# Kernel optimization log

Hardware: AMD Instinct MI355X
Metric: run time of the kernel (lower is better)

The kernel has to match this reference:

```python
import jax, jax.numpy as jnp
import numpy as np

DIM = 768
NUM_EXPERTS = 1536
EXPERT_DIM = 64
NOISE_SCALE = 0.1
B, H, W = 1, 64, 64
N = B * H * W


def setup_inputs() -> dict:
    key = jax.random.key(0)
    ks = jax.random.split(key, 6)
    scaled = lambda k, shape, fan_in: (jax.random.normal(k, shape, jnp.float32) / np.sqrt(fan_in)).astype(jnp.float32)
    return {
        "x": jax.random.normal(ks[0], (B, H, W, DIM), jnp.float32),
        "noise": jax.random.normal(ks[1], (N, NUM_EXPERTS), jnp.float32),
        "gate_w": scaled(ks[2], (NUM_EXPERTS, DIM), DIM),
        "gate_b": jnp.zeros((NUM_EXPERTS,), jnp.float32),
        "expert_w": scaled(ks[3], (NUM_EXPERTS, EXPERT_DIM, DIM), DIM),  # torch Linear weight layout (out, in)
        "expert_b": jnp.zeros((NUM_EXPERTS, EXPERT_DIM), jnp.float32),
        "proj_w": scaled(ks[4], (DIM, EXPERT_DIM), EXPERT_DIM),
        "proj_b": jnp.zeros((DIM,), jnp.float32),
    }


def reference(x, noise, gate_w, gate_b, expert_w, expert_b, proj_w, proj_b):
    orig_shape = x.shape
    xf = x.reshape(-1, orig_shape[-1])  # (N, DIM)
    # Noisy gating
    scores = xf @ gate_w.T + gate_b + noise * NOISE_SCALE  # (N, E)
    gate_weights = jax.nn.softmax(scores, axis=-1)
    top_w, top_i = jax.lax.top_k(gate_weights, 1)  # (N, 1), (N, 1)
    idx = top_i[:, 0]  # (N,)
    # Gather only the selected expert per token (same math as the redundant
    # dense all-expert compute followed by a gather in the original).
    w_sel = expert_w[idx]  # (N, EXPERT_DIM, DIM)
    b_sel = expert_b[idx]  # (N, EXPERT_DIM)
    y = jnp.einsum('nd,nod->no', xf, w_sel) + b_sel  # (N, EXPERT_DIM)
    out_flat = (y @ proj_w.T + proj_b) * top_w  # (N, DIM); top_w broadcasts (N,1)
    return out_flat.reshape(orig_shape)
```

## Files before the change

kernel.cpp:

```cpp
#include <hip/hip_runtime.h>
#include <hip/hip_bf16.h>

#define NT 4096
#define DIM 768
#define NE 1536
#define ED 64
#define GAP_THR 8e-3f
#define MAXG 2304

typedef __attribute__((ext_vector_type(8))) short short8v;
typedef __attribute__((ext_vector_type(4))) float f32x4;

__device__ __forceinline__ unsigned short f2bf(float f) {
  unsigned int u = __float_as_uint(f);
  unsigned int r = (u + 0x7fffu + ((u >> 16) & 1u)) >> 16;
  return (unsigned short)r;
}
__device__ __forceinline__ float bf2f(unsigned short h) {
  return __uint_as_float(((unsigned int)h) << 16);
}

__device__ __forceinline__ void gload16(const void* g, void* l) {
  __builtin_amdgcn_global_load_lds((const __attribute__((address_space(1))) void*)g,
                                   (__attribute__((address_space(3))) void*)l, 16, 0, 0);
}

__device__ __forceinline__ void top2_merge(float& m1, int& i1, float& m2, int& i2,
                                           float om1, int oi1, float om2, int oi2) {
  if (om1 > m1 || (om1 == m1 && oi1 < i1)) {
    if (m1 > om2 || (m1 == om2 && i1 < oi2)) { m2 = m1; i2 = i1; }
    else { m2 = om2; i2 = oi2; }
    m1 = om1; i1 = oi1;
  } else {
    if (om1 > m2 || (om1 == m2 && oi1 < i2)) { m2 = om1; i2 = oi1; }
  }
}

__global__ __launch_bounds__(256) void split_all(
    const float* __restrict__ x, const float* __restrict__ gw,
    unsigned short* __restrict__ xhi, unsigned short* __restrict__ xlo,
    unsigned short* __restrict__ ghi, unsigned short* __restrict__ glo,
    int* __restrict__ rc_cnt, int* __restrict__ counts) {
  if (blockIdx.x == 0) {
    for (int j = threadIdx.x; j < NE; j += 256) counts[j] = 0;
    if (threadIdx.x == 0) *rc_cnt = 0;
  }
  const int nx4 = NT * DIM / 4;
  const int ng4 = NE * DIM / 4;
  int i = blockIdx.x * 256 + threadIdx.x;
  const float* src; unsigned short* hi; unsigned short* lo; int j;
  if (i < nx4) { src = x; hi = xhi; lo = xlo; j = i; }
  else { j = i - nx4; if (j >= ng4) return; src = gw; hi = ghi; lo = glo; }
  float4 v = ((const float4*)src)[j];
  unsigned short h0 = f2bf(v.x), h1 = f2bf(v.y), h2 = f2bf(v.z), h3 = f2bf(v.w);
  ((ushort4*)hi)[j] = make_ushort4(h0, h1, h2, h3);
  ((ushort4*)lo)[j] = make_ushort4(f2bf(v.x - bf2f(h0)), f2bf(v.y - bf2f(h1)),
                                   f2bf(v.z - bf2f(h2)), f2bf(v.w - bf2f(h3)));
}

__global__ __launch_bounds__(256) void gate_mfma(
    const unsigned short* __restrict__ xhi, const unsigned short* __restrict__ xlo,
    const unsigned short* __restrict__ ghi, const unsigned short* __restrict__ glo,
    const float* __restrict__ gb, const float* __restrict__ noise,
    float4* __restrict__ part_a, int* __restrict__ part_i2) {
  __shared__ __align__(16) unsigned short sA[2 * 64 * 32];
  __shared__ __align__(16) unsigned short sB[2 * 128 * 32];
  const int tid = threadIdx.x;
  const int w = tid >> 6, lane = tid & 63;
  const int bm = blockIdx.x, bn = blockIdx.y;
  const int fr = lane & 15;
  const int fg = lane >> 4;
  const int gsw = fg ^ ((fr >> 1) & 3);

  f32x4 acc[4][2];
#pragma unroll
  for (int i = 0; i < 4; i++)
#pragma unroll
    for (int j = 0; j < 2; j++) acc[i][j] = (f32x4){0.f, 0.f, 0.f, 0.f};

  const size_t arow = (size_t)bm * 64 * DIM;
  const size_t brow = (size_t)bn * 128 * DIM;
  const int rA = tid >> 2;
  const int sgA = (tid & 3) ^ ((rA >> 1) & 3);
  const int sgB = (tid & 3) ^ ((tid >> 3) & 3);

  for (int kt = 0; kt < DIM; kt += 32) {
    __syncthreads();
    {
      const size_t asrc = arow + (size_t)rA * DIM + kt + sgA * 8;
      gload16(xhi + asrc, &sA[w * 512]);
      gload16(xlo + asrc, &sA[2048 + w * 512]);
#pragma unroll
      for (int h = 0; h < 2; h++) {
        const int r = h * 64 + (tid >> 2);
        const size_t bsrc = brow + (size_t)r * DIM + kt + sgB * 8;
        gload16(ghi + bsrc, &sB[h * 2048 + w * 512]);
        gload16(glo + bsrc, &sB[4096 + h * 2048 + w * 512]);
      }
    }
    __syncthreads();

    short8v ah[4], al[4], bh[2], bl[2];
#pragma unroll
    for (int mf = 0; mf < 4; mf++) {
      int ro = (mf * 16 + fr) * 32 + gsw * 8;
      ah[mf] = *(const short8v*)&sA[ro];
      al[mf] = *(const short8v*)&sA[2048 + ro];
    }
#pragma unroll
    for (int nf = 0; nf < 2; nf++) {
      int ro = (w * 32 + nf * 16 + fr) * 32 + gsw * 8;
      bh[nf] = *(const short8v*)&sB[ro];
      bl[nf] = *(const short8v*)&sB[4096 + ro];
    }
#pragma unroll
    for (int mf = 0; mf < 4; mf++)
#pragma unroll
      for (int nf = 0; nf < 2; nf++) {
        f32x4 c = acc[mf][nf];
        c = __builtin_amdgcn_mfma_f32_16x16x32_bf16(ah[mf], bh[nf], c, 0, 0, 0);
        c = __builtin_amdgcn_mfma_f32_16x16x32_bf16(ah[mf], bl[nf], c, 0, 0, 0);
        c = __builtin_amdgcn_mfma_f32_16x16x32_bf16(al[mf], bh[nf], c, 0, 0, 0);
        acc[mf][nf] = c;
      }
  }

  const int gm0 = bm * 64;
  const int gn0 = bn * 128 + w * 32;
  const int chunk = bn * 4 + w;
  int gcol[2]; float gbv[2];
#pragma unroll
  for (int nf = 0; nf < 2; nf++) { gcol[nf] = gn0 + nf * 16 + fr; gbv[nf] = gb[gcol[nf]]; }
#pragma unroll
  for (int mf = 0; mf < 4; mf++) {
    float sv[2][4];
#pragma unroll
    for (int nf = 0; nf < 2; nf++)
#pragma unroll
      for (int reg = 0; reg < 4; reg++) {
        int gm = gm0 + mf * 16 + fg * 4 + reg;
        sv[nf][reg] = acc[mf][nf][reg] + gbv[nf] + 0.1f * noise[(size_t)gm * NE + gcol[nf]];
      }
#pragma unroll
    for (int reg = 0; reg < 4; reg++) {
      float m1 = sv[0][reg]; int i1 = gcol[0];
      float m2 = -3e38f; int i2 = 0x7fffffff;
      {
        float v = sv[1][reg]; int ii = gcol[1];
        if (v > m1 || (v == m1 && ii < i1)) { m2 = m1; i2 = i1; m1 = v; i1 = ii; }
        else { m2 = v; i2 = ii; }
      }
#pragma unroll
      for (int off = 1; off <= 8; off <<= 1) {
        float om1 = __shfl_xor(m1, off, 64); int oi1 = __shfl_xor(i1, off, 64);
        float om2 = __shfl_xor(m2, off, 64); int oi2 = __shfl_xor(i2, off, 64);
        top2_merge(m1, i1, m2, i2, om1, oi1, om2, oi2);
      }
      float ssum = __expf(sv[0][reg] - m1) + __expf(sv[1][reg] - m1);
#pragma unroll
      for (int off = 1; off <= 8; off <<= 1) ssum += __shfl_xor(ssum, off, 64);
      if (fr == 0) {
        int gm = gm0 + mf * 16 + fg * 4 + reg;
        part_a[(size_t)gm * 48 + chunk] = make_float4(m1, m2, ssum, __int_as_float(i1));
        part_i2[(size_t)gm * 48 + chunk] = i2;
      }
    }
  }
}

__global__ __launch_bounds__(256) void finalize(
    const float4* __restrict__ part_a, const int* __restrict__ part_i2,
    float* __restrict__ topw, int* __restrict__ idx, int* __restrict__ counts,
    int* __restrict__ rc_count, int* __restrict__ rc_n, int* __restrict__ rc_i2) {
  const int wv = threadIdx.x >> 6, lane = threadIdx.x & 63;
  const int n = blockIdx.x * 4 + wv;
  float m1 = -3e38f, m2 = -3e38f, lm1 = -3e38f, lsum = 0.f;
  int i1 = 0x7fffffff, i2 = 0x7fffffff;
  if (lane < 48) {
    float4 pa = part_a[(size_t)n * 48 + lane];
    m1 = pa.x; m2 = pa.y; lsum = pa.z; i1 = __float_as_int(pa.w);
    i2 = part_i2[(size_t)n * 48 + lane];
    lm1 = pa.x;
  }
#pragma unroll
  for (int off = 1; off <= 32; off <<= 1) {
    float om1 = __shfl_xor(m1, off, 64); int oi1 = __shfl_xor(i1, off, 64);
    float om2 = __shfl_xor(m2, off, 64); int oi2 = __shfl_xor(i2, off, 64);
    top2_merge(m1, i1, m2, i2, om1, oi1, om2, oi2);
  }
  float contrib = (lane < 48) ? __expf(lm1 - m1) * lsum : 0.f;
#pragma unroll
  for (int off = 1; off <= 32; off <<= 1) contrib += __shfl_xor(contrib, off, 64);
  if (lane == 0) {
    topw[n] = 1.0f / contrib;
    idx[n] = i1;
    atomicAdd(counts + i1, 1);
    if (m1 - m2 < GAP_THR) {
      int p = atomicAdd(rc_count, 1);
      rc_n[p] = n; rc_i2[p] = i2;
    }
  }
}

__global__ __launch_bounds__(256) void recheck(
    const float* __restrict__ x, const float* __restrict__ gw,
    const float* __restrict__ gb, const float* __restrict__ noise,
    const int* __restrict__ rc_n, const int* __restrict__ rc_i2,
    const int* __restrict__ rc_count, int* __restrict__ idx, int* __restrict__ counts) {
  __shared__ float r1[4], r2[4];
  const int cnt = *rc_count;
  const int tid = threadIdx.x;
  const int w = tid >> 6, lane = tid & 63;
  for (int t = blockIdx.x; t < cnt; t += gridDim.x) {
    const int n = rc_n[t];
    const int e1 = idx[n], e2 = rc_i2[t];
    const float* xr = x + (size_t)n * DIM;
    const float* w1 = gw + (size_t)e1 * DIM;
    const float* w2 = gw + (size_t)e2 * DIM;
    float p1 = 0.f, p2 = 0.f;
    for (int k = tid; k < DIM; k += 256) {
      float xv = xr[k];
      p1 += xv * w1[k];
      p2 += xv * w2[k];
    }
#pragma unroll
    for (int off = 32; off; off >>= 1) {
      p1 += __shfl_xor(p1, off, 64);
      p2 += __shfl_xor(p2, off, 64);
    }
    if (lane == 0) { r1[w] = p1; r2[w] = p2; }
    __syncthreads();
    if (tid == 0) {
      float s1 = r1[0] + r1[1] + r1[2] + r1[3] + gb[e1] + 0.1f * noise[(size_t)n * NE + e1];
      float s2 = r2[0] + r2[1] + r2[2] + r2[3] + gb[e2] + 0.1f * noise[(size_t)n * NE + e2];
      if (s2 > s1 || (s2 == s1 && e2 < e1)) {
        idx[n] = e2;
        atomicSub(counts + e1, 1);
        atomicAdd(counts + e2, 1);
      }
    }
    __syncthreads();
  }
}

__global__ __launch_bounds__(256) void scan_offsets(
    const int* __restrict__ counts, int* __restrict__ offs, int* __restrict__ cursor,
    int* __restrict__ gdesc, int* __restrict__ ngroups) {
  __shared__ int part[256];
  __shared__ int part2[256];
  const int t = threadIdx.x;
  int loc[6];
  int s = 0, s2 = 0;
#pragma unroll
  for (int j = 0; j < 6; j++) {
    loc[j] = counts[t * 6 + j];
    s += loc[j];
    s2 += (loc[j] + 3) >> 2;
  }
  part[t] = s; part2[t] = s2;
  __syncthreads();
  for (int d = 1; d < 256; d <<= 1) {
    int v1 = (t >= d) ? part[t - d] : 0;
    int v2 = (t >= d) ? part2[t - d] : 0;
    __syncthreads();
    part[t] += v1; part2[t] += v2;
    __syncthreads();
  }
  int excl = part[t] - s;
  int excl2 = part2[t] - s2;
#pragma unroll
  for (int j = 0; j < 6; j++) {
    const int e = t * 6 + j, c = loc[j];
    offs[e] = excl;
    cursor[e] = excl;
    const int ng = (c + 3) >> 2;
    for (int k = 0; k < ng; k++) {
      gdesc[3 * (excl2 + k)]     = e;
      gdesc[3 * (excl2 + k) + 1] = excl + 4 * k;
      gdesc[3 * (excl2 + k) + 2] = min(4, c - 4 * k);
    }
    excl += c; excl2 += ng;
  }
  if (t == 255) *ngroups = part2[255];
}

__global__ __launch_bounds__(256) void scatter_tokens(
    const int* __restrict__ idx, int* __restrict__ cursor, int* __restrict__ sorted) {
  const int n = blockIdx.x * 256 + threadIdx.x;
  int e = idx[n];
  int pos = atomicAdd(cursor + e, 1);
  sorted[pos] = n;
}

__global__ __launch_bounds__(256) void expert_y(
    const float* __restrict__ x, const float* __restrict__ ew,
    const float* __restrict__ eb, const int* __restrict__ sorted,
    const int* __restrict__ gdesc, const int* __restrict__ ngroups,
    float* __restrict__ y) {
  const int g = blockIdx.x;
  if (g >= *ngroups) return;
  const int e    = gdesc[3 * g];
  const int base = gdesc[3 * g + 1];
  const int cc   = gdesc[3 * g + 2];
  const int tid = threadIdx.x;
  const int w = tid >> 6, lane = tid & 63;

  const int tk0 = sorted[base];
  const int tk1 = sorted[base + (1 < cc ? 1 : 0)];
  const int tk2 = sorted[base + (2 < cc ? 2 : 0)];
  const int tk3 = sorted[base + (3 < cc ? 3 : 0)];
  const int mytk = (lane == 0) ? tk0 : (lane == 1) ? tk1 : (lane == 2) ? tk2 : tk3;

  const float4* W4 = (const float4*)(ew + (size_t)e * ED * DIM);
  const float4* X4 = (const float4*)x;
  const float4* Wc = W4 + w * 16 * 192;

  f32x4 x00 = *(const f32x4*)&X4[(size_t)tk0 * 192 + lane];
  f32x4 x01 = *(const f32x4*)&X4[(size_t)tk0 * 192 + 64 + lane];
  f32x4 x02 = *(const f32x4*)&X4[(size_t)tk0 * 192 + 128 + lane];
  f32x4 x10 = *(const f32x4*)&X4[(size_t)tk1 * 192 + lane];
  f32x4 x11 = *(const f32x4*)&X4[(size_t)tk1 * 192 + 64 + lane];
  f32x4 x12 = *(const f32x4*)&X4[(size_t)tk1 * 192 + 128 + lane];
  f32x4 x20 = *(const f32x4*)&X4[(size_t)tk2 * 192 + lane];
  f32x4 x21 = *(const f32x4*)&X4[(size_t)tk2 * 192 + 64 + lane];
  f32x4 x22 = *(const f32x4*)&X4[(size_t)tk2 * 192 + 128 + lane];
  f32x4 x30 = *(const f32x4*)&X4[(size_t)tk3 * 192 + lane];
  f32x4 x31 = *(const f32x4*)&X4[(size_t)tk3 * 192 + 64 + lane];
  f32x4 x32 = *(const f32x4*)&X4[(size_t)tk3 * 192 + 128 + lane];

  f32x4 wbuf[2][3];
#pragma unroll
  for (int j = 0; j < 3; j++) wbuf[0][j] = *(const f32x4*)&Wc[j * 64 + lane];
#pragma unroll
  for (int j = 0; j < 3; j++) wbuf[1][j] = *(const f32x4*)&Wc[192 + j * 64 + lane];

#pragma unroll
  for (int a = 0; a < 16; a++) {
    const int cur = a & 1;
    f32x4 wa0 = wbuf[cur][0], wa1 = wbuf[cur][1], wa2 = wbuf[cur][2];
    if (a < 14) {
      wbuf[cur][0] = *(const f32x4*)&Wc[(a + 2) * 192 + lane];
      wbuf[cur][1] = *(const f32x4*)&Wc[(a + 2) * 192 + 64 + lane];
      wbuf[cur][2] = *(const f32x4*)&Wc[(a + 2) * 192 + 128 + lane];
    }
    float p0 = wa0.x * x00.x + wa0.y * x00.y + wa0.z * x00.z + wa0.w * x00.w
             + wa1.x * x01.x + wa1.y * x01.y + wa1.z * x01.z + wa1.w * x01.w
             + wa2.x * x02.x + wa2.y * x02.y + wa2.z * x02.z + wa2.w * x02.w;
    float p1 = wa0.x * x10.x + wa0.y * x10.y + wa0.z * x10.z + wa0.w * x10.w
             + wa1.x * x11.x + wa1.y * x11.y + wa1.z * x11.z + wa1.w * x11.w
             + wa2.x * x12.x + wa2.y * x12.y + wa2.z * x12.z + wa2.w * x12.w;
    float p2 = wa0.x * x20.x + wa0.y * x20.y + wa0.z * x20.z + wa0.w * x20.w
             + wa1.x * x21.x + wa1.y * x21.y + wa1.z * x21.z + wa1.w * x21.w
             + wa2.x * x22.x + wa2.y * x22.y + wa2.z * x22.z + wa2.w * x22.w;
    float p3 = wa0.x * x30.x + wa0.y * x30.y + wa0.z * x30.z + wa0.w * x30.w
             + wa1.x * x31.x + wa1.y * x31.y + wa1.z * x31.z + wa1.w * x31.w
             + wa2.x * x32.x + wa2.y * x32.y + wa2.z * x32.z + wa2.w * x32.w;

    const bool b0 = (lane & 1) != 0;
    float q0 = (b0 ? p1 : p0) + __shfl_xor(b0 ? p0 : p1, 1, 64);
    float q1 = (b0 ? p3 : p2) + __shfl_xor(b0 ? p2 : p3, 1, 64);
    const bool b1 = (lane & 2) != 0;
    float r = (b1 ? q1 : q0) + __shfl_xor(b1 ? q0 : q1, 2, 64);
    r += __shfl_xor(r, 4, 64);
    r += __shfl_xor(r, 8, 64);
    r += __shfl_xor(r, 16, 64);
    r += __shfl_xor(r, 32, 64);

    const int o = w * 16 + a;
    if (lane < cc) {
      y[(size_t)mytk * ED + o] = r + eb[e * ED + o];
    }
  }
}

__global__ __launch_bounds__(256) void proj_kernel(
    const float* __restrict__ y, const float* __restrict__ pw,
    const float* __restrict__ pb, const float* __restrict__ topw,
    float* __restrict__ out) {
  const int b = blockIdx.x;
  const int tid = threadIdx.x;
  __shared__ float4 ys4[8 * 16];
  __shared__ float tw[8];
  if (tid < 128) {
    int t = tid >> 4, q = tid & 15;
    ys4[tid] = ((const float4*)y)[((size_t)b * 8 + t) * 16 + q];
  }
  if (tid < 8) tw[tid] = topw[b * 8 + tid];
  __syncthreads();
  const float4* pw4 = (const float4*)pw;
#pragma unroll
  for (int c = 0; c < 3; c++) {
    int d = c * 256 + tid;
    float4 pwv[16];
#pragma unroll
    for (int q = 0; q < 16; q++) pwv[q] = pw4[(size_t)d * 16 + q];
    float pbv = pb[d];
    for (int t = 0; t < 8; t++) {
      const float4* yv4 = &ys4[t * 16];
      float s = 0.f;
#pragma unroll
      for (int q = 0; q < 16; q++) {
        float4 yv = yv4[q];
        s += pwv[q].x * yv.x + pwv[q].y * yv.y + pwv[q].z * yv.z + pwv[q].w * yv.w;
      }
      out[((size_t)b * 8 + t) * DIM + d] = (s + pbv) * tw[t];
    }
  }
}

extern "C" void kernel_launch(void* const* d_in, const int* in_sizes, int n_in,
                              void* d_out, int out_size, void* d_ws, size_t ws_size,
                              hipStream_t stream) {
  const float* x      = (const float*)d_in[0];
  const float* noise  = (const float*)d_in[1];
  const float* gate_w = (const float*)d_in[2];
  const float* gate_b = (const float*)d_in[3];
  const float* ew     = (const float*)d_in[4];
  const float* eb     = (const float*)d_in[5];
  const float* pw     = (const float*)d_in[6];
  const float* pb     = (const float*)d_in[7];
  float* out = (float*)d_out;

  char* ws = (char*)d_ws;
  unsigned short* xhi    = (unsigned short*)(ws);
  unsigned short* xlo    = (unsigned short*)(ws + 6291456);
  unsigned short* ghi    = (unsigned short*)(ws + 12582912);
  unsigned short* glo    = (unsigned short*)(ws + 14942208);
  float4*         part_a = (float4*)(ws + 17301504);
  int*            part_i2= (int*)  (ws + 20447232);
  float*          y      = (float*)(ws + 21233664);
  float*          topw   = (float*)(ws + 22282240);
  int*            idx    = (int*)  (ws + 22298624);
  int*            counts = (int*)  (ws + 22315008);
  int*            rc_cnt = (int*)  (ws + 22321152);
  int*            offs   = (int*)  (ws + 22321408);
  int*            cursor = (int*)  (ws + 22327552);
  int*            sorted = (int*)  (ws + 22333696);
  int*            rc_n   = (int*)  (ws + 22350080);
  int*            rc_i2  = (int*)  (ws + 22366464);
  int*            ngroups= (int*)  (ws + 22382848);
  int*            gdesc  = (int*)  (ws + 22383104);

  split_all<<<(NT * DIM / 4 + NE * DIM / 4 + 255) / 256, 256, 0, stream>>>(
      x, gate_w, xhi, xlo, ghi, glo, rc_cnt, counts);
  gate_mfma<<<dim3(NT / 64, NE / 128), 256, 0, stream>>>(
      xhi, xlo, ghi, glo, gate_b, noise, part_a, part_i2);
  finalize<<<NT / 4, 256, 0, stream>>>(part_a, part_i2, topw, idx, counts,
                                       rc_cnt, rc_n, rc_i2);
  recheck<<<64, 256, 0, stream>>>(x, gate_w, gate_b, noise, rc_n, rc_i2, rc_cnt,
                                  idx, counts);
  scan_offsets<<<1, 256, 0, stream>>>(counts, offs, cursor, gdesc, ngroups);
  scatter_tokens<<<NT / 256, 256, 0, stream>>>(idx, cursor, sorted);
  expert_y<<<MAXG, 256, 0, stream>>>(x, ew, eb, sorted, gdesc, ngroups, y);
  proj_kernel<<<NT / 8, 256, 0, stream>>>(y, pw, pb, topw, out);
}
```

Baseline: 232.4 us.

## Use fp16 split gate GEMM with double-buffered LDS and fused scan/scatter

The gate GEMM now uses fp16: x is stored as a single fp16 copy and gate_w as an fp16 hi/lo pair. This cuts the split-precision MFMAs from three to two per fragment and removes the x low-part buffer traffic. The K loop double-buffers LDS so the next tile loads while the current one computes, with one barrier per iteration. The scan_offsets and scatter_tokens kernels are merged into one single-block kernel that uses LDS atomics, removing one launch. The risks are fp16 range and precision loss on x, which the recheck gap threshold must absorb, and a serial scatter running on only one block.

```diff
diff --git a/kernel.cpp b/kernel.cpp
--- a/kernel.cpp
+++ b/kernel.cpp
@@ -8,17 +8,9 @@
 #define GAP_THR 8e-3f
 #define MAXG 2304
 
-typedef __attribute__((ext_vector_type(8))) short short8v;
+typedef __attribute__((ext_vector_type(8))) _Float16 half8v;
+typedef __attribute__((ext_vector_type(4))) _Float16 half4v;
 typedef __attribute__((ext_vector_type(4))) float f32x4;
-
-__device__ __forceinline__ unsigned short f2bf(float f) {
-  unsigned int u = __float_as_uint(f);
-  unsigned int r = (u + 0x7fffu + ((u >> 16) & 1u)) >> 16;
-  return (unsigned short)r;
-}
-__device__ __forceinline__ float bf2f(unsigned short h) {
-  return __uint_as_float(((unsigned int)h) << 16);
-}
 
 __device__ __forceinline__ void gload16(const void* g, void* l) {
   __builtin_amdgcn_global_load_lds((const __attribute__((address_space(1))) void*)g,
@@ -38,8 +30,7 @@
 
 __global__ __launch_bounds__(256) void split_all(
     const float* __restrict__ x, const float* __restrict__ gw,
-    unsigned short* __restrict__ xhi, unsigned short* __restrict__ xlo,
-    unsigned short* __restrict__ ghi, unsigned short* __restrict__ glo,
+    _Float16* __restrict__ xh, _Float16* __restrict__ gh, _Float16* __restrict__ gl,
     int* __restrict__ rc_cnt, int* __restrict__ counts) {
   if (blockIdx.x == 0) {
     for (int j = threadIdx.x; j < NE; j += 256) counts[j] = 0;
@@ -48,28 +39,34 @@
   const int nx4 = NT * DIM / 4;
   const int ng4 = NE * DIM / 4;
   int i = blockIdx.x * 256 + threadIdx.x;
-  const float* src; unsigned short* hi; unsigned short* lo; int j;
-  if (i < nx4) { src = x; hi = xhi; lo = xlo; j = i; }
-  else { j = i - nx4; if (j >= ng4) return; src = gw; hi = ghi; lo = glo; }
-  float4 v = ((const float4*)src)[j];
-  unsigned short h0 = f2bf(v.x), h1 = f2bf(v.y), h2 = f2bf(v.z), h3 = f2bf(v.w);
-  ((ushort4*)hi)[j] = make_ushort4(h0, h1, h2, h3);
-  ((ushort4*)lo)[j] = make_ushort4(f2bf(v.x - bf2f(h0)), f2bf(v.y - bf2f(h1)),
-                                   f2bf(v.z - bf2f(h2)), f2bf(v.w - bf2f(h3)));
+  if (i < nx4) {
+    float4 v = ((const float4*)x)[i];
+    half4v hv = {(_Float16)v.x, (_Float16)v.y, (_Float16)v.z, (_Float16)v.w};
+    ((half4v*)xh)[i] = hv;
+  } else {
+    int j = i - nx4;
+    if (j >= ng4) return;
+    float4 v = ((const float4*)gw)[j];
+    half4v hv = {(_Float16)v.x, (_Float16)v.y, (_Float16)v.z, (_Float16)v.w};
+    half4v lv = {(_Float16)(v.x - (float)hv[0]), (_Float16)(v.y - (float)hv[1]),
+                 (_Float16)(v.z - (float)hv[2]), (_Float16)(v.w - (float)hv[3])};
+    ((half4v*)gh)[j] = hv;
+    ((half4v*)gl)[j] = lv;
+  }
 }
 
 __global__ __launch_bounds__(256) void gate_mfma(
-    const unsigned short* __restrict__ xhi, const unsigned short* __restrict__ xlo,
-    const unsigned short* __restrict__ ghi, const unsigned short* __restrict__ glo,
-    const float* __restrict__ gb, const float* __restrict__ noise,
-    float4* __restrict__ part_a, int* __restrict__ part_i2) {
-  __shared__ __align__(16) unsigned short sA[2 * 64 * 32];
-  __shared__ __align__(16) unsigned short sB[2 * 128 * 32];
+    const _Float16* __restrict__ xh, const _Float16* __restrict__ gh,
+    const _Float16* __restrict__ gl, const float* __restrict__ gb,
+    const float* __restrict__ noise, float4* __restrict__ part_a,
+    int* __restrict__ part_i2) {
+  __shared__ __align__(16) _Float16 sA[2][64 * 32];
+  __shared__ __align__(16) _Float16 sBh[2][128 * 32];
+  __shared__ __align__(16) _Float16 sBl[2][128 * 32];
   const int tid = threadIdx.x;
   const int w = tid >> 6, lane = tid & 63;
   const int bm = blockIdx.x, bn = blockIdx.y;
-  const int fr = lane & 15;
-  const int fg = lane >> 4;
+  const int fr = lane & 15, fg = lane >> 4;
   const int gsw = fg ^ ((fr >> 1) & 3);
 
   f32x4 acc[4][2];
@@ -81,49 +78,47 @@
   const size_t arow = (size_t)bm * 64 * DIM;
   const size_t brow = (size_t)bn * 128 * DIM;
   const int rA = tid >> 2;
-  const int sgA = (tid & 3) ^ ((rA >> 1) & 3);
-  const int sgB = (tid & 3) ^ ((tid >> 3) & 3);
-
-  for (int kt = 0; kt < DIM; kt += 32) {
-    __syncthreads();
-    {
-      const size_t asrc = arow + (size_t)rA * DIM + kt + sgA * 8;
-      gload16(xhi + asrc, &sA[w * 512]);
-      gload16(xlo + asrc, &sA[2048 + w * 512]);
-#pragma unroll
-      for (int h = 0; h < 2; h++) {
-        const int r = h * 64 + (tid >> 2);
-        const size_t bsrc = brow + (size_t)r * DIM + kt + sgB * 8;
-        gload16(ghi + bsrc, &sB[h * 2048 + w * 512]);
-        gload16(glo + bsrc, &sB[4096 + h * 2048 + w * 512]);
-      }
-    }
-    __syncthreads();
-
-    short8v ah[4], al[4], bh[2], bl[2];
-#pragma unroll
-    for (int mf = 0; mf < 4; mf++) {
-      int ro = (mf * 16 + fr) * 32 + gsw * 8;
-      ah[mf] = *(const short8v*)&sA[ro];
-      al[mf] = *(const short8v*)&sA[2048 + ro];
-    }
+  const int sg = (tid & 3) ^ ((rA >> 1) & 3);
+  const int dA = w * 512;
+
+#define STAGE(b, kt) do {                                                     \
+    gload16(xh + arow + (size_t)rA * DIM + (kt) + sg * 8, &sA[b][dA]);        \
+    gload16(gh + brow + (size_t)rA * DIM + (kt) + sg * 8, &sBh[b][dA]);       \
+    gload16(gl + brow + (size_t)rA * DIM + (kt) + sg * 8, &sBl[b][dA]);       \
+    gload16(gh + brow + (size_t)(64 + rA) * DIM + (kt) + sg * 8, &sBh[b][2048 + dA]); \
+    gload16(gl + brow + (size_t)(64 + rA) * DIM + (kt) + sg * 8, &sBl[b][2048 + dA]); \
+  } while (0)
+
+  STAGE(0, 0);
+  __syncthreads();
+
+  for (int t = 0; t < 24; t++) {
+    const int cur = t & 1;
+    if (t < 23) {
+      if (cur) STAGE(0, (t + 1) * 32); else STAGE(1, (t + 1) * 32);
+    }
+    half8v a8[4], b8h[2], b8l[2];
+#pragma unroll
+    for (int mf = 0; mf < 4; mf++)
+      a8[mf] = *(const half8v*)&sA[cur][(mf * 16 + fr) * 32 + gsw * 8];
 #pragma unroll
     for (int nf = 0; nf < 2; nf++) {
       int ro = (w * 32 + nf * 16 + fr) * 32 + gsw * 8;
-      bh[nf] = *(const short8v*)&sB[ro];
-      bl[nf] = *(const short8v*)&sB[4096 + ro];
+      b8h[nf] = *(const half8v*)&sBh[cur][ro];
+      b8l[nf] = *(const half8v*)&sBl[cur][ro];
     }
 #pragma unroll
     for (int mf = 0; mf < 4; mf++)
 #pragma unroll
       for (int nf = 0; nf < 2; nf++) {
         f32x4 c = acc[mf][nf];
-        c = __builtin_amdgcn_mfma_f32_16x16x32_bf16(ah[mf], bh[nf], c, 0, 0, 0);
-        c = __builtin_amdgcn_mfma_f32_16x16x32_bf16(ah[mf], bl[nf], c, 0, 0, 0);
-        c = __builtin_amdgcn_mfma_f32_16x16x32_bf16(al[mf], bh[nf], c, 0, 0, 0);
+        c = __builtin_amdgcn_mfma_f32_16x16x32_f16(a8[mf], b8h[nf], c, 0, 0, 0);
+        c = __builtin_amdgcn_mfma_f32_16x16x32_f16(a8[mf], b8l[nf], c, 0, 0, 0);
         acc[mf][nf] = c;
       }
-  }
+    __syncthreads();
+  }
+#undef STAGE
 
   const int gm0 = bm * 64;
   const int gn0 = bn * 128 + w * 32;
@@ -243,11 +238,12 @@
   }
 }
 
-__global__ __launch_bounds__(256) void scan_offsets(
-    const int* __restrict__ counts, int* __restrict__ offs, int* __restrict__ cursor,
-    int* __restrict__ gdesc, int* __restrict__ ngroups) {
+__global__ __launch_bounds__(256) void sortscan(
+    const int* __restrict__ counts, const int* __restrict__ idx,
+    int* __restrict__ sorted, int* __restrict__ gdesc, int* __restrict__ ngroups) {
   __shared__ int part[256];
   __shared__ int part2[256];
+  __shared__ int lcur[NE];
   const int t = threadIdx.x;
   int loc[6];
   int s = 0, s2 = 0;
@@ -271,8 +267,7 @@
 #pragma unroll
   for (int j = 0; j < 6; j++) {
     const int e = t * 6 + j, c = loc[j];
-    offs[e] = excl;
-    cursor[e] = excl;
+    lcur[e] = excl;
     const int ng = (c + 3) >> 2;
     for (int k = 0; k < ng; k++) {
       gdesc[3 * (excl2 + k)]     = e;
@@ -282,14 +277,12 @@
     excl += c; excl2 += ng;
   }
   if (t == 255) *ngroups = part2[255];
-}
-
-__global__ __launch_bounds__(256) void scatter_tokens(
-    const int* __restrict__ idx, int* __restrict__ cursor, int* __restrict__ sorted) {
-  const int n = blockIdx.x * 256 + threadIdx.x;
-  int e = idx[n];
-  int pos = atomicAdd(cursor + e, 1);
-  sorted[pos] = n;
+  __syncthreads();
+  for (int n = t; n < NT; n += 256) {
+    int e = idx[n];
+    int pos = atomicAdd(&lcur[e], 1);
+    sorted[pos] = n;
+  }
 }
 
 __global__ __launch_bounds__(256) void expert_y(
@@ -422,35 +415,31 @@
   float* out = (float*)d_out;
 
   char* ws = (char*)d_ws;
-  unsigned short* xhi    = (unsigned short*)(ws);
-  unsigned short* xlo    = (unsigned short*)(ws + 6291456);
-  unsigned short* ghi    = (unsigned short*)(ws + 12582912);
-  unsigned short* glo    = (unsigned short*)(ws + 14942208);
-  float4*         part_a = (float4*)(ws + 17301504);
-  int*            part_i2= (int*)  (ws + 20447232);
-  float*          y      = (float*)(ws + 21233664);
-  float*          topw   = (float*)(ws + 22282240);
-  int*            idx    = (int*)  (ws + 22298624);
-  int*            counts = (int*)  (ws + 22315008);
-  int*            rc_cnt = (int*)  (ws + 22321152);
-  int*            offs   = (int*)  (ws + 22321408);
-  int*            cursor = (int*)  (ws + 22327552);
-  int*            sorted = (int*)  (ws + 22333696);
-  int*            rc_n   = (int*)  (ws + 22350080);
-  int*            rc_i2  = (int*)  (ws + 22366464);
-  int*            ngroups= (int*)  (ws + 22382848);
-  int*            gdesc  = (int*)  (ws + 22383104);
+  _Float16* xh     = (_Float16*)(ws);
+  _Float16* gh     = (_Float16*)(ws + 6291456);
+  _Float16* gl     = (_Float16*)(ws + 8650752);
+  float4*   part_a = (float4*)(ws + 11010048);
+  int*      part_i2= (int*)   (ws + 14155776);
+  float*    y      = (float*)  (ws + 14942208);
+  float*    topw   = (float*)  (ws + 15990784);
+  int*      idx    = (int*)    (ws + 16007168);
+  int*      counts = (int*)    (ws + 16023552);
+  int*      rc_cnt = (int*)    (ws + 16029696);
+  int*      sorted = (int*)    (ws + 16029952);
+  int*      rc_n   = (int*)    (ws + 16046336);
+  int*      rc_i2  = (int*)    (ws + 16062720);
+  int*      ngroups= (int*)    (ws + 16079104);
+  int*      gdesc  = (int*)    (ws + 16079360);
 
   split_all<<<(NT * DIM / 4 + NE * DIM / 4 + 255) / 256, 256, 0, stream>>>(
-      x, gate_w, xhi, xlo, ghi, glo, rc_cnt, counts);
+      x, gate_w, xh, gh, gl, rc_cnt, counts);
   gate_mfma<<<dim3(NT / 64, NE / 128), 256, 0, stream>>>(
-      xhi, xlo, ghi, glo, gate_b, noise, part_a, part_i2);
+      xh, gh, gl, gate_b, noise, part_a, part_i2);
   finalize<<<NT / 4, 256, 0, stream>>>(part_a, part_i2, topw, idx, counts,
                                        rc_cnt, rc_n, rc_i2);
   recheck<<<64, 256, 0, stream>>>(x, gate_w, gate_b, noise, rc_n, rc_i2, rc_cnt,
                                   idx, counts);
-  scan_offsets<<<1, 256, 0, stream>>>(counts, offs, cursor, gdesc, ngroups);
-  scatter_tokens<<<NT / 256, 256, 0, stream>>>(idx, cursor, sorted);
+  sortscan<<<1, 256, 0, stream>>>(counts, idx, sorted, gdesc, ngroups);
   expert_y<<<MAXG, 256, 0, stream>>>(x, ew, eb, sorted, gdesc, ngroups, y);
   proj_kernel<<<NT / 8, 256, 0, stream>>>(y, pw, pb, topw, out);
 }
```

Result: faster. 225.4 us (-3.0%).
